# Kernel tuning notes

Hardware: AMD Instinct MI355X
Metric: run time of the kernel (lower is better)

## Reference

```python
import jax, jax.numpy as jnp
import numpy as np
from jax import lax

SCORE_THRESHOLD = 0.5
IOU_THRESHOLD = 0.5
IMG_SIZE = 640.0
SPLITTER_THRESHOLD = 0.0
N = 4096


def setup_inputs() -> dict:
    key = jax.random.key(0)
    # raw RT-DETR output: [1, N, 5] = (cx, cy, w, h, person_conf), all in [0, 1]
    rtdetr_raw_out = jax.random.uniform(key, (1, N, 5), dtype=jnp.float32)
    return {"rtdetr_raw_out": rtdetr_raw_out}


def _iou_matrix(boxes):
    # boxes: [N, 4] in xyxy. Returns [N, N] pairwise IoU.
    x1, y1, x2, y2 = boxes[:, 0], boxes[:, 1], boxes[:, 2], boxes[:, 3]
    area = (x2 - x1) * (y2 - y1)  # [N]
    ix1 = jnp.maximum(x1[:, None], x1[None, :])
    iy1 = jnp.maximum(y1[:, None], y1[None, :])
    ix2 = jnp.minimum(x2[:, None], x2[None, :])
    iy2 = jnp.minimum(y2[:, None], y2[None, :])
    iw = jnp.clip(ix2 - ix1, 0.0)
    ih = jnp.clip(iy2 - iy1, 0.0)
    inter = iw * ih
    union = area[:, None] + area[None, :] - inter
    return inter / jnp.maximum(union, 1e-9)


def reference(rtdetr_raw_out):
    raw = rtdetr_raw_out[0]  # squeeze(0) -> [N, 5]
    conf = raw[:, 4]
    # splitter: keep boxes with conf > 0.0 (expressed as a mask for fixed shapes)
    valid = conf > SPLITTER_THRESHOLD
    # cxcywh scaled to pixel coords, then converted to xyxy
    cxcywh = raw[:, :4] * IMG_SIZE
    cx, cy, w, h = cxcywh[:, 0], cxcywh[:, 1], cxcywh[:, 2], cxcywh[:, 3]
    xyxy = jnp.stack([cx - w * 0.5, cy - h * 0.5, cx + w * 0.5, cy + h * 0.5], axis=1)
    # NMS score filter: conf >= score_threshold
    valid = valid & (conf >= SCORE_THRESHOLD)
    # sort by score descending; invalid boxes sink to the bottom with -inf keys
    sort_key = jnp.where(valid, conf, -jnp.inf)
    order = jnp.argsort(-sort_key)
    boxes_s = xyxy[order]          # [N, 4]
    conf_s = conf[order]           # [N]
    valid_s = valid[order]         # [N]
    iou = _iou_matrix(boxes_s)     # [N, N]
    idx = jnp.arange(N)

    def body(i, keep):
        keep_i = keep[i]
        # suppress any lower-ranked box with IoU > threshold to a kept box i
        sup = (iou[i] > IOU_THRESHOLD) & keep_i & (idx > i)
        return keep & (~sup)

    keep = lax.fori_loop(0, N, body, valid_s)
    boxes_and_scores = jnp.concatenate([boxes_s, conf_s[:, None]], axis=1)  # [N, 5]
    # fixed-shape equivalent of boolean-gather: suppressed/invalid rows zeroed
    return boxes_and_scores * keep[:, None].astype(boxes_and_scores.dtype)
```

## Files before the change

### kernel.cpp

```cpp
#include <hip/hip_runtime.h>
#include <stdint.h>

#define NBOX 4096
#define IMG 640.0f

typedef unsigned long long u64;
typedef unsigned int u32;


__global__ __launch_bounds__(256) void k_rank(const float* __restrict__ raw,
                                              int* __restrict__ rank_partial, int* __restrict__ Mp) {
    const int bi = blockIdx.x, bj = blockIdx.y;
    const int t = threadIdx.x;
    const int i = bi * 256 + t;
    if (bi == 0 && bj == 0 && t == 0) *Mp = 0;
    __shared__ float cj[256];
    cj[t] = raw[(bj * 256 + t) * 5 + 4];
    __syncthreads();

    const float ci = raw[i * 5 + 4];
    const int jbase = bj * 256;
    int rank = 0;
    const float4* c4 = reinterpret_cast<const float4*>(cj);
#pragma unroll 4
    for (int j4 = 0; j4 < 64; ++j4) {
        float4 c = c4[j4];
        int j = jbase + j4 * 4;
        rank += (c.x > ci || (c.x == ci && (j + 0) < i)) ? 1 : 0;
        rank += (c.y > ci || (c.y == ci && (j + 1) < i)) ? 1 : 0;
        rank += (c.z > ci || (c.z == ci && (j + 2) < i)) ? 1 : 0;
        rank += (c.w > ci || (c.w == ci && (j + 3) < i)) ? 1 : 0;
    }
    rank_partial[bj * NBOX + i] = rank;
}

__global__ __launch_bounds__(256) void k_scatter(const float* __restrict__ raw,
                                                 const int* __restrict__ rank_partial,
                                                 float* __restrict__ sx1, float* __restrict__ sy1,
                                                 float* __restrict__ sx2, float* __restrict__ sy2,
                                                 float* __restrict__ sconf, int* __restrict__ Mp) {
    const int i = blockIdx.x * 256 + threadIdx.x;
    const float ci = raw[i * 5 + 4];
    const bool vi = (ci >= 0.5f);

    int rank = 0;
#pragma unroll
    for (int k = 0; k < 16; ++k) rank += rank_partial[k * NBOX + i];

    u64 bal = __ballot(vi);
    if ((threadIdx.x & 63) == 0) atomicAdd(Mp, (int)__popcll(bal));

    if (vi) {
        float cx = __fmul_rn(raw[i * 5 + 0], IMG);
        float cy = __fmul_rn(raw[i * 5 + 1], IMG);
        float w  = __fmul_rn(raw[i * 5 + 2], IMG);
        float h  = __fmul_rn(raw[i * 5 + 3], IMG);
        float hw = __fmul_rn(w, 0.5f);
        float hh = __fmul_rn(h, 0.5f);
        sx1[rank]   = __fsub_rn(cx, hw);
        sy1[rank]   = __fsub_rn(cy, hh);
        sx2[rank]   = __fadd_rn(cx, hw);
        sy2[rank]   = __fadd_rn(cy, hh);
        sconf[rank] = ci;
    }
}

__global__ __launch_bounds__(256) void k_mask(const float* __restrict__ sx1, const float* __restrict__ sy1,
                                              const float* __restrict__ sx2, const float* __restrict__ sy2,
                                              const int* __restrict__ Mp,
                                              u64* __restrict__ mask, u64* __restrict__ diagR) {
    const int w = blockIdx.y;
    const int r = blockIdx.x * 256 + threadIdx.x;
    const int t = threadIdx.x;
    const int M = *Mp;

    __shared__ float cx1[64], cy1[64], cx2[64], cy2[64], car[64];
    if (t < 64) {
        int j = (w << 6) + t;
        float a1 = sx1[j], b1 = sy1[j], a2 = sx2[j], b2 = sy2[j];
        cx1[t] = a1; cy1[t] = b1; cx2[t] = a2; cy2[t] = b2;
        car[t] = __fmul_rn(__fsub_rn(a2, a1), __fsub_rn(b2, b1));
    }
    __syncthreads();

    u64 bits = 0ULL;
    if (r < M) {
        const float x1 = sx1[r], y1 = sy1[r], x2 = sx2[r], y2 = sy2[r];
        const float area_i = __fmul_rn(__fsub_rn(x2, x1), __fsub_rn(y2, y1));
        const int bmax = min(64, M - (w << 6));
        const int bmin = max(0, r + 1 - (w << 6));
        for (int b = bmin; b < bmax; ++b) {
            float xx1 = fmaxf(x1, cx1[b]);
            float yy1 = fmaxf(y1, cy1[b]);
            float xx2 = fminf(x2, cx2[b]);
            float yy2 = fminf(y2, cy2[b]);
            float iw = fmaxf(__fsub_rn(xx2, xx1), 0.0f);
            float ih = fmaxf(__fsub_rn(yy2, yy1), 0.0f);
            float inter = __fmul_rn(iw, ih);
            float uni = __fsub_rn(__fadd_rn(area_i, car[b]), inter);
            float iou = __fdiv_rn(inter, fmaxf(uni, 1e-9f));
            if (iou > 0.5f) bits |= (1ULL << b);
        }
        mask[((size_t)r << 6) + w] = bits;
    }

    if ((r >> 6) == w) diagR[r] = bits;
}

__global__ __launch_bounds__(576) void k_scan(const int* __restrict__ Mp,
                                              const u64* __restrict__ mask,
                                              const u64* __restrict__ diagR,
                                              u64* __restrict__ keepw) {
    __shared__ u64 remvArr[64];
    __shared__ u64 kbArr[64];
    const int tid = threadIdx.x;
    const int wave = tid >> 6;
    const int lane = tid & 63;
    const int M = *Mp;
    const int nblk = (M + 63) >> 6;
    if (nblk == 0) return;

    if (tid < 64) remvArr[tid] = 0ULL;

    if (wave == 0) {
        __builtin_amdgcn_s_setprio(1);
        u64 rv = diagR[lane];
        u32 rlo = (u32)rv, rhi = (u32)(rv >> 32);
        u64 colv = (nblk > 1) ? mask[((size_t)lane << 6) + 1] : 0ULL;
        u64 carry = 0ULL;

        for (int b = 0; b < nblk; ++b) {
            u64 rb = remvArr[b];
            const int rem = M - (b << 6);
            const u64 valid = (rem >= 64) ? ~0ULL : ((1ULL << rem) - 1ULL);
            u64 alive = valid & ~(rb | carry);
            u64 kb = 0ULL;
            while (alive) {
                int i = __builtin_ctzll(alive);
                alive &= alive - 1;
                kb |= (1ULL << i);
                u32 lo = __builtin_amdgcn_readlane(rlo, i);
                u32 hi = __builtin_amdgcn_readlane(rhi, i);
                alive &= ~(((u64)hi << 32) | (u64)lo);
            }
            if (lane == 0) { kbArr[b] = kb; keepw[b] = kb; }

            u64 nc = ((kb >> lane) & 1ULL) ? colv : 0ULL;
            nc |= __shfl_xor(nc, 1);
            nc |= __shfl_xor(nc, 2);
            nc |= __shfl_xor(nc, 4);
            nc |= __shfl_xor(nc, 8);
            nc |= __shfl_xor(nc, 16);
            nc |= __shfl_xor(nc, 32);
            carry = nc;

            if (b + 1 < nblk) {
                u64 nrv = diagR[((b + 1) << 6) + lane];
                rlo = (u32)nrv; rhi = (u32)(nrv >> 32);
                colv = (b + 2 < nblk)
                     ? mask[(((size_t)(b + 1) << 6) + lane) * 64 + (b + 2)]
                     : 0ULL;
            }
            asm volatile("s_waitcnt lgkmcnt(0)" ::: "memory");
            __builtin_amdgcn_s_barrier();
            __builtin_amdgcn_sched_barrier(0);
        }
    } else {
        const int w1 = wave - 1;
        const int slot = tid & 7;
        const int chunk = (tid >> 3) & 7;
        for (int b = 0; b < nblk; ++b) {
            if (b >= 1) {
                const u64 kb = kbArr[b - 1];
                const int W = b + 1 + (w1 << 3) + slot;
                if (kb != 0ULL && W < 64) {
                    const u64* rowbase = mask + ((size_t)(b - 1) << 12);
                    u64 acc = 0ULL;
#pragma unroll
                    for (int k = 0; k < 8; ++k) {
                        const int r = chunk + (k << 3);
                        u64 v = rowbase[((size_t)r << 6) + W];
                        acc |= (((kb >> r) & 1ULL) ? v : 0ULL);
                    }
                    acc |= __shfl_xor(acc, 8);
                    acc |= __shfl_xor(acc, 16);
                    acc |= __shfl_xor(acc, 32);
                    if (chunk == 0) remvArr[W] |= acc;
                }
            }
            asm volatile("s_waitcnt lgkmcnt(0)" ::: "memory");
            __builtin_amdgcn_s_barrier();
            __builtin_amdgcn_sched_barrier(0);
        }
    }
}

__global__ __launch_bounds__(256) void k_out(const float* __restrict__ sx1, const float* __restrict__ sy1,
                                             const float* __restrict__ sx2, const float* __restrict__ sy2,
                                             const float* __restrict__ sconf,
                                             const int* __restrict__ Mp,
                                             const u64* __restrict__ keepw,
                                             float* __restrict__ out) {
    const int g = blockIdx.x * 256 + threadIdx.x;
    if (g >= NBOX * 5) return;
    const int r = g / 5;
    const int c = g - r * 5;
    const int M = *Mp;
    bool kept = false;
    if (r < M) kept = ((keepw[r >> 6] >> (r & 63)) & 1ULL) != 0ULL;
    float v = 0.0f;
    if (kept) {
        const float* arr = (c == 0) ? sx1 : (c == 1) ? sy1 : (c == 2) ? sx2 : (c == 3) ? sy2 : sconf;
        v = arr[r];
    }
    out[g] = v;
}

extern "C" void kernel_launch(void* const* d_in, const int* in_sizes, int n_in,
                              void* d_out, int out_size, void* d_ws, size_t ws_size,
                              hipStream_t stream) {
    const float* raw = (const float*)d_in[0];
    char* ws = (char*)d_ws;
    float* sx1 = (float*)(ws + 0);
    float* sy1 = (float*)(ws + 16384);
    float* sx2 = (float*)(ws + 32768);
    float* sy2 = (float*)(ws + 49152);
    float* sconf = (float*)(ws + 65536);
    int* Mp = (int*)(ws + 81920);
    u64* keepw = (u64*)(ws + 82432);
    u64* diagR = (u64*)(ws + 86016);
    u64* mask = (u64*)(ws + 131072);
    int* rank_partial = (int*)(ws + 2228224);
    float* out = (float*)d_out;

    k_rank<<<dim3(16, 16), dim3(256), 0, stream>>>(raw, rank_partial, Mp);
    k_scatter<<<dim3(16), dim3(256), 0, stream>>>(raw, rank_partial, sx1, sy1, sx2, sy2, sconf, Mp);
    k_mask<<<dim3(16, 64), dim3(256), 0, stream>>>(sx1, sy1, sx2, sy2, Mp, mask, diagR);
    k_scan<<<dim3(1), dim3(576), 0, stream>>>(Mp, mask, diagR, keepw);
    k_out<<<dim3(80), dim3(256), 0, stream>>>(sx1, sy1, sx2, sy2, sconf, Mp, keepw, out);
}
```

Baseline: 91.62 us.

## Fuse output kernel into scan, prefetch mask rows, and compute carry via readlane

Folds the output-writing kernel into the single-block scan kernel, using the kept bits held in shared memory and dropping one launch and the keep-word global round trip. The serial wave now builds the next-block carry inside the greedy loop with readlanes instead of a six-step shuffle reduction. Helper waves prefetch the next block's mask rows into registers one iteration early so the loads overlap the serial work. The trade-off is that the output write (20K floats) now runs on a single workgroup instead of 80 blocks.

```diff
diff --git a/kernel.cpp b/kernel.cpp
--- a/kernel.cpp
+++ b/kernel.cpp
@@ -110,7 +110,10 @@
 __global__ __launch_bounds__(576) void k_scan(const int* __restrict__ Mp,
                                               const u64* __restrict__ mask,
                                               const u64* __restrict__ diagR,
-                                              u64* __restrict__ keepw) {
+                                              const float* __restrict__ sx1, const float* __restrict__ sy1,
+                                              const float* __restrict__ sx2, const float* __restrict__ sy2,
+                                              const float* __restrict__ sconf,
+                                              float* __restrict__ out) {
     __shared__ u64 remvArr[64];
     __shared__ u64 kbArr[64];
     const int tid = threadIdx.x;
@@ -118,102 +121,101 @@
     const int lane = tid & 63;
     const int M = *Mp;
     const int nblk = (M + 63) >> 6;
-    if (nblk == 0) return;
-
-    if (tid < 64) remvArr[tid] = 0ULL;
-
-    if (wave == 0) {
-        __builtin_amdgcn_s_setprio(1);
-        u64 rv = diagR[lane];
-        u32 rlo = (u32)rv, rhi = (u32)(rv >> 32);
-        u64 colv = (nblk > 1) ? mask[((size_t)lane << 6) + 1] : 0ULL;
-        u64 carry = 0ULL;
-
-        for (int b = 0; b < nblk; ++b) {
-            u64 rb = remvArr[b];
-            const int rem = M - (b << 6);
-            const u64 valid = (rem >= 64) ? ~0ULL : ((1ULL << rem) - 1ULL);
-            u64 alive = valid & ~(rb | carry);
-            u64 kb = 0ULL;
-            while (alive) {
-                int i = __builtin_ctzll(alive);
-                alive &= alive - 1;
-                kb |= (1ULL << i);
-                u32 lo = __builtin_amdgcn_readlane(rlo, i);
-                u32 hi = __builtin_amdgcn_readlane(rhi, i);
-                alive &= ~(((u64)hi << 32) | (u64)lo);
+
+    if (tid < 64) { remvArr[tid] = 0ULL; kbArr[tid] = 0ULL; }
+
+    if (nblk > 0) {
+        if (wave == 0) {
+            __builtin_amdgcn_s_setprio(1);
+            u64 rv = diagR[lane];
+            u32 rlo = (u32)rv, rhi = (u32)(rv >> 32);
+            u64 cv = (nblk > 1) ? mask[((size_t)lane << 6) + 1] : 0ULL;
+            u32 clo = (u32)cv, chi = (u32)(cv >> 32);
+            u64 carry = 0ULL;
+
+            for (int b = 0; b < nblk; ++b) {
+                u64 rb = remvArr[b];
+                const int rem = M - (b << 6);
+                const u64 valid = (rem >= 64) ? ~0ULL : ((1ULL << rem) - 1ULL);
+                u64 alive = valid & ~(rb | carry);
+                u64 kb = 0ULL, car = 0ULL;
+                while (alive) {
+                    int i = __builtin_ctzll(alive);
+                    alive &= alive - 1;
+                    kb |= (1ULL << i);
+                    u32 lo = __builtin_amdgcn_readlane(rlo, i);
+                    u32 hi = __builtin_amdgcn_readlane(rhi, i);
+                    u32 cl = __builtin_amdgcn_readlane(clo, i);
+                    u32 ch = __builtin_amdgcn_readlane(chi, i);
+                    alive &= ~(((u64)hi << 32) | (u64)lo);
+                    car |= (((u64)ch << 32) | (u64)cl);
+                }
+                carry = car;
+                if (lane == 0) kbArr[b] = kb;
+
+                if (b + 1 < nblk) {
+                    u64 nrv = diagR[((b + 1) << 6) + lane];
+                    rlo = (u32)nrv; rhi = (u32)(nrv >> 32);
+                    u64 ncv = (b + 2 < nblk)
+                            ? mask[(((size_t)(b + 1) << 6) + lane) * 64 + (b + 2)]
+                            : 0ULL;
+                    clo = (u32)ncv; chi = (u32)(ncv >> 32);
+                }
+                asm volatile("s_waitcnt lgkmcnt(0)" ::: "memory");
+                __builtin_amdgcn_s_barrier();
+                __builtin_amdgcn_sched_barrier(0);
             }
-            if (lane == 0) { kbArr[b] = kb; keepw[b] = kb; }
-
-            u64 nc = ((kb >> lane) & 1ULL) ? colv : 0ULL;
-            nc |= __shfl_xor(nc, 1);
-            nc |= __shfl_xor(nc, 2);
-            nc |= __shfl_xor(nc, 4);
-            nc |= __shfl_xor(nc, 8);
-            nc |= __shfl_xor(nc, 16);
-            nc |= __shfl_xor(nc, 32);
-            carry = nc;
-
-            if (b + 1 < nblk) {
-                u64 nrv = diagR[((b + 1) << 6) + lane];
-                rlo = (u32)nrv; rhi = (u32)(nrv >> 32);
-                colv = (b + 2 < nblk)
-                     ? mask[(((size_t)(b + 1) << 6) + lane) * 64 + (b + 2)]
-                     : 0ULL;
-            }
-            asm volatile("s_waitcnt lgkmcnt(0)" ::: "memory");
-            __builtin_amdgcn_s_barrier();
-            __builtin_amdgcn_sched_barrier(0);
-        }
-    } else {
-        const int w1 = wave - 1;
-        const int slot = tid & 7;
-        const int chunk = (tid >> 3) & 7;
-        for (int b = 0; b < nblk; ++b) {
-            if (b >= 1) {
-                const u64 kb = kbArr[b - 1];
-                const int W = b + 1 + (w1 << 3) + slot;
-                if (kb != 0ULL && W < 64) {
-                    const u64* rowbase = mask + ((size_t)(b - 1) << 12);
-                    u64 acc = 0ULL;
+        } else {
+            const int w1 = wave - 1;
+            const int slot = tid & 7;
+            const int chunk = (tid >> 3) & 7;
+            u64 v[8];
+            for (int b = 0; b < nblk; ++b) {
+                if (b >= 1) {
+                    const u64 kb = kbArr[b - 1];
+                    const int W = b + 1 + (w1 << 3) + slot;
+                    if (kb != 0ULL && W < 64) {
+                        u64 acc = 0ULL;
+#pragma unroll
+                        for (int k = 0; k < 8; ++k) {
+                            const int r = chunk + (k << 3);
+                            acc |= (((kb >> r) & 1ULL) ? v[k] : 0ULL);
+                        }
+                        acc |= __shfl_xor(acc, 8);
+                        acc |= __shfl_xor(acc, 16);
+                        acc |= __shfl_xor(acc, 32);
+                        if (chunk == 0) remvArr[W] |= acc;
+                    }
+                }
+                if (b + 1 < nblk) {
+                    const int W2 = b + 2 + (w1 << 3) + slot;
+                    const int Wc = (W2 < 64) ? W2 : 63;
+                    const u64* rowbase = mask + ((size_t)b << 12);
 #pragma unroll
                     for (int k = 0; k < 8; ++k) {
                         const int r = chunk + (k << 3);
-                        u64 v = rowbase[((size_t)r << 6) + W];
-                        acc |= (((kb >> r) & 1ULL) ? v : 0ULL);
+                        v[k] = rowbase[((size_t)r << 6) + Wc];
                     }
-                    acc |= __shfl_xor(acc, 8);
-                    acc |= __shfl_xor(acc, 16);
-                    acc |= __shfl_xor(acc, 32);
-                    if (chunk == 0) remvArr[W] |= acc;
-                }
+                }
+                asm volatile("s_waitcnt lgkmcnt(0)" ::: "memory");
+                __builtin_amdgcn_s_barrier();
+                __builtin_amdgcn_sched_barrier(0);
             }
-            asm volatile("s_waitcnt lgkmcnt(0)" ::: "memory");
-            __builtin_amdgcn_s_barrier();
-            __builtin_amdgcn_sched_barrier(0);
         }
     }
-}
-
-__global__ __launch_bounds__(256) void k_out(const float* __restrict__ sx1, const float* __restrict__ sy1,
-                                             const float* __restrict__ sx2, const float* __restrict__ sy2,
-                                             const float* __restrict__ sconf,
-                                             const int* __restrict__ Mp,
-                                             const u64* __restrict__ keepw,
-                                             float* __restrict__ out) {
-    const int g = blockIdx.x * 256 + threadIdx.x;
-    if (g >= NBOX * 5) return;
-    const int r = g / 5;
-    const int c = g - r * 5;
-    const int M = *Mp;
-    bool kept = false;
-    if (r < M) kept = ((keepw[r >> 6] >> (r & 63)) & 1ULL) != 0ULL;
-    float v = 0.0f;
-    if (kept) {
-        const float* arr = (c == 0) ? sx1 : (c == 1) ? sy1 : (c == 2) ? sx2 : (c == 3) ? sy2 : sconf;
-        v = arr[r];
-    }
-    out[g] = v;
+    if (nblk == 0) __builtin_amdgcn_s_barrier();
+    for (int g = tid; g < NBOX * 5; g += 576) {
+        const int r = g / 5;
+        const int c = g - r * 5;
+        bool kept = false;
+        if (r < M) kept = ((kbArr[r >> 6] >> (r & 63)) & 1ULL) != 0ULL;
+        float vv = 0.0f;
+        if (kept) {
+            const float* arr = (c == 0) ? sx1 : (c == 1) ? sy1 : (c == 2) ? sx2 : (c == 3) ? sy2 : sconf;
+            vv = arr[r];
+        }
+        out[g] = vv;
+    }
 }
 
 extern "C" void kernel_launch(void* const* d_in, const int* in_sizes, int n_in,
@@ -227,7 +229,6 @@
     float* sy2 = (float*)(ws + 49152);
     float* sconf = (float*)(ws + 65536);
     int* Mp = (int*)(ws + 81920);
-    u64* keepw = (u64*)(ws + 82432);
     u64* diagR = (u64*)(ws + 86016);
     u64* mask = (u64*)(ws + 131072);
     int* rank_partial = (int*)(ws + 2228224);
@@ -236,6 +237,5 @@
     k_rank<<<dim3(16, 16), dim3(256), 0, stream>>>(raw, rank_partial, Mp);
     k_scatter<<<dim3(16), dim3(256), 0, stream>>>(raw, rank_partial, sx1, sy1, sx2, sy2, sconf, Mp);
     k_mask<<<dim3(16, 64), dim3(256), 0, stream>>>(sx1, sy1, sx2, sy2, Mp, mask, diagR);
-    k_scan<<<dim3(1), dim3(576), 0, stream>>>(Mp, mask, diagR, keepw);
-    k_out<<<dim3(80), dim3(256), 0, stream>>>(sx1, sy1, sx2, sy2, sconf, Mp, keepw, out);
-}
+    k_scan<<<dim3(1), dim3(576), 0, stream>>>(Mp, mask, diagR, sx1, sy1, sx2, sy2, sconf, out);
+}
```

After: 87.40 us. -4.6%, faster.
